# Optimization experiments

Measured on AMD Instinct MI355X. Metric: run time of the kernel, lower is better.

## Reference

```python
import jax, jax.numpy as jnp
import numpy as np

N, D, B, E = 3072, 64, 12, 49152


def _gat_conv(x, mask, W, a_src, a_dst, b):
    # PyG GATConv (eval mode): per-edge score = LeakyReLU(a_dst.Wx_i + a_src.Wx_j),
    # softmax over incoming neighbors (mask includes self-loops), concat heads.
    H, d = a_src.shape
    h = (x @ W).reshape(x.shape[0], H, d)                  # [N, H, d]
    es = jnp.einsum('nhd,hd->nh', h, a_src)                # source-side score
    ed = jnp.einsum('nhd,hd->nh', h, a_dst)                # dest-side score
    e = jax.nn.leaky_relu(ed[:, None, :] + es[None, :, :], 0.2)  # [Ndst, Nsrc, H]
    e = jnp.where(mask[:, :, None], e, -jnp.inf)
    alpha = jax.nn.softmax(e, axis=1)                      # softmax over sources
    out = jnp.einsum('ijh,jhd->ihd', alpha, h)
    return out.reshape(x.shape[0], H * d) + b


def _gcn_conv(x, Abool, W, b):
    # PyG GCNConv: add self-loops, symmetric deg^{-1/2} normalization.
    n = x.shape[0]
    Ahat = Abool.astype(x.dtype) + jnp.eye(n, dtype=x.dtype)
    deg = Ahat.sum(1)
    dinv = jnp.where(deg > 0, 1.0 / jnp.sqrt(deg), 0.0)
    return (dinv[:, None] * Ahat * dinv[None, :]) @ (x @ W) + b


def _forward(x, ei, g1_W, g1_as, g1_ad, g1_b, g2_W, g2_as, g2_ad, g2_b,
             gA_W, gA_b, gB_W, gB_b, gC_W, gC_b, c2_W, c2_b, c3_W, c3_b,
             hwA_W, hwA_b, hwB_W, hwB_b, gru_Wih, gru_Whh, gru_bih, gru_bhh,
             tA_W, tA_b, tB_W, tB_b, edge_index, atom_list, res_list):
    n = x.shape[0]
    relu = jax.nn.relu
    I = jnp.eye(n, dtype=bool)
    # A[dst, src] = 1 (PyG messages flow src -> dst); ei only sets to_dense_adj
    # values in the original, which are never used (only adj.shape).
    A = jnp.zeros((n, n), dtype=bool).at[edge_index[1], edge_index[0]].set(True)
    Af = A.astype(x.dtype)
    A2 = (Af @ Af) > 0                      # spspmm(E, E): 2-hop edges
    A3 = (Af @ A2.astype(x.dtype)) > 0      # spspmm(E^2, E): 3-hop edges
    counts = atom_list + res_list
    batch = jnp.repeat(jnp.arange(counts.shape[0]), counts, total_repeat_length=n)

    def gat_block(mask):
        v = jax.nn.elu(_gat_conv(x, mask, g1_W, g1_as, g1_ad, g1_b))
        v = relu(_gat_conv(v, mask, g2_W, g2_as, g2_ad, g2_b))
        v = relu(v @ gA_W + gA_b)
        v = relu(v @ gB_W + gB_b)
        return v @ gC_W + gC_b

    h1 = relu(gat_block(A | I))
    h1 = relu(_gcn_conv(h1, A, c2_W, c2_b))
    h1 = relu(_gcn_conv(h1, A, c3_W, c3_b))          # [N, 4D]
    h2 = relu(gat_block(A2 | I))
    h2 = relu(_gcn_conv(h2, A2, c2_W, c2_b))          # [N, 2D]
    h3 = relu(gat_block(A3 | I))                      # [N, D]
    # HighWay fusion
    bb = h2 @ hwB_W + hwB_b
    aa = h1 @ hwA_W + hwA_b
    z = jax.nn.sigmoid(aa + bb)
    hh = z * bb + (1.0 - z) * aa
    # GRUCell(input=h3, hidden=hh), PyTorch gate order r, z, n
    gx = h3 @ gru_Wih + gru_bih
    gh = hh @ gru_Whh + gru_bhh
    xr, xz, xn = jnp.split(gx, 3, axis=1)
    hr, hz, hn = jnp.split(gh, 3, axis=1)
    r = jax.nn.sigmoid(xr + hr)
    zz = jax.nn.sigmoid(xz + hz)
    nn_ = jnp.tanh(xn + r * hn)
    cc = (1.0 - zz) * nn_ + zz * hh
    vi = jax.ops.segment_max(cc, batch, num_segments=atom_list.shape[0])  # global_max_pool
    vi = relu(vi @ tA_W + tA_b)
    return vi @ tB_W + tB_b


def setup_inputs() -> dict:
    key = jax.random.key(0)
    ks = jax.random.split(key, 40)
    it = iter(range(40))

    def p(shp):
        return jax.random.normal(ks[next(it)], shp, dtype=jnp.float32) * 0.1

    src = jax.random.randint(ks[next(it)], (E,), 0, N)
    dst = jax.random.randint(ks[next(it)], (E,), 0, N)
    dst = jnp.where(dst == src, (dst + 1) % N, dst)   # no self-loops in raw edges
    edge_index = jnp.stack([src, dst])
    inp = {
        'x': jax.random.normal(ks[next(it)], (N, D), dtype=jnp.float32),
        'ei': jax.random.uniform(ks[next(it)], (E,), dtype=jnp.float32),
        'g1_W': p((D, 8 * D)), 'g1_as': p((8, D)), 'g1_ad': p((8, D)), 'g1_b': p((8 * D,)),
        'g2_W': p((8 * D, D)), 'g2_as': p((1, D)), 'g2_ad': p((1, D)), 'g2_b': p((D,)),
        'gA_W': p((D, D)), 'gA_b': p((D,)), 'gB_W': p((D, 128)), 'gB_b': p((128,)),
        'gC_W': p((128, D)), 'gC_b': p((D,)),
        'c2_W': p((D, 2 * D)), 'c2_b': p((2 * D,)), 'c3_W': p((2 * D, 4 * D)), 'c3_b': p((4 * D,)),
        'hwA_W': p((4 * D, D)), 'hwA_b': p((D,)), 'hwB_W': p((2 * D, D)), 'hwB_b': p((D,)),
        'gru_Wih': p((D, 3 * D)), 'gru_Whh': p((D, 3 * D)), 'gru_bih': p((3 * D,)), 'gru_bhh': p((3 * D,)),
        'tA_W': p((D, 128)), 'tA_b': p((128,)), 'tB_W': p((128, 120)), 'tB_b': p((120,)),
        'edge_index': edge_index,
        'atom_list': jnp.full((B,), 156, dtype=jnp.int32),
        'res_list': jnp.full((B,), 100, dtype=jnp.int32),
    }
    return inp


def reference(x, ei, g1_W, g1_as, g1_ad, g1_b, g2_W, g2_as, g2_ad, g2_b,
              gA_W, gA_b, gB_W, gB_b, gC_W, gC_b, c2_W, c2_b, c3_W, c3_b,
              hwA_W, hwA_b, hwB_W, hwB_b, gru_Wih, gru_Whh, gru_bih, gru_bhh,
              tA_W, tA_b, tB_W, tB_b, edge_index, atom_list, res_list):
    return _forward(x, ei, g1_W, g1_as, g1_ad, g1_b, g2_W, g2_as, g2_ad, g2_b,
                    gA_W, gA_b, gB_W, gB_b, gC_W, gC_b, c2_W, c2_b, c3_W, c3_b,
                    hwA_W, hwA_b, hwB_W, hwB_b, gru_Wih, gru_Whh, gru_bih, gru_bhh,
                    tA_W, tA_b, tB_W, tB_b, edge_index, atom_list, res_list)
```

## Files before the change

kernel.cpp:

```cpp
#include <hip/hip_runtime.h>
#include <math.h>

namespace {

constexpr int NN = 3072;
constexpr int NW = 96;
constexpr int NEDGE_C = 49152;
constexpr int NB = 12;
constexpr float RLN2 = 1.44269504088896340736f;

using short8v = __attribute__((ext_vector_type(8))) short;
using f32x4v  = __attribute__((ext_vector_type(4))) float;
typedef unsigned short ushort_t;

__device__ __forceinline__ float leaky02(float x) { return fmaxf(x, 0.2f * x); }
__device__ __forceinline__ float sigm(float x) { return 1.f / (1.f + __expf(-x)); }

__device__ __forceinline__ float hi_part(float a) {
  return __uint_as_float(__float_as_uint(a) & 0xffff0000u);
}
__device__ __forceinline__ unsigned pack_h(float a, float b) {
  return (__float_as_uint(a) >> 16) | (__float_as_uint(b) & 0xffff0000u);
}
__device__ __forceinline__ unsigned pack_l(float a, float b) {
// ... 175 lines not shown
                                           unsigned* jlist, int* cnt, int t) {
  if (t < 16) {
    int base = 0;
    for (int k = 0; k < t; ++k) base += __popc(rowb[p * 16 + k]);
    unsigned m = rowb[p * 16 + t];
    int j0 = p * 512 + t * 32;
    while (m) { int b = __ffs(m) - 1; m &= m - 1; jlist[base++] = j0 + b; }
    if (t == 15) *cnt = base;
  }
  __syncthreads();
  return *cnt;
}

template<int JS>
__global__ __launch_bounds__(256) void k_gat_sparse8_part(
    const float* __restrict__ hsrc,
    const float* __restrict__ es,
    const float* __restrict__ ed,
    const float* __restrict__ gm,
    const unsigned* __restrict__ bits,
    float* __restrict__ pacc,
    float* __restrict__ pden) {
  constexpr int WPS = NW / JS;
  constexpr int WPP = WPS / 2;
  __shared__ unsigned rowb[WPS];
  __shared__ unsigned jlist[WPP * 32];
  __shared__ float wl[WPP * 32 * 8];
  __shared__ int cnt;
  __shared__ float red[256];
  int i = blockIdx.x, z = blockIdx.y, t = threadIdx.x;
  int w0 = z * WPS;
  if (t < WPS) {
    unsigned wv_ = bits[(size_t)i * NW + w0 + t];
    if (w0 + t == (i >> 5)) wv_ |= 1u << (i & 31);
    rowb[t] = wv_;
  }
  int wv = t >> 6, lane = t & 63;
  int ha = lane >> 4;
  int hb = 4 + (lane >> 4);
  int ca = lane * 4;
  float4 a0 = {0.f, 0.f, 0.f, 0.f};
  float4 a1 = {0.f, 0.f, 0.f, 0.f};
  int hw = t & 7;
  float edv = ed[(size_t)i * 8 + hw];
  float mh = leaky02(edv + gm[hw]);
  float dloc = 0.f;
  __syncthreads();

  for (int p = 0; p < 2; ++p) {
    __syncthreads();
    if (t < WPP) {
      int base = 0;
      for (int k = p * WPP; k < p * WPP + t; ++k) base += __popc(rowb[k]);
      unsigned m = rowb[p * WPP + t];
      int j0 = (w0 + p * WPP + t) * 32;
      while (m) { int b = __ffs(m) - 1; m &= m - 1; jlist[base++] = j0 + b; }
      if (t == WPP - 1) cnt = base;
    }
    __syncthreads();
    int c = cnt;
    if (c == 0) continue;
    for (int pidx = t; pidx < c * 8; pidx += 256) {
      int idx = pidx >> 3;
      int j = (int)jlist[idx];
      float w = exp2f(leaky02(edv + es[(size_t)j * 8 + hw]) - mh);
      wl[idx * 8 + hw] = w;
      dloc += w;
    }
    __syncthreads();
    int idx = wv;
    for (; idx + 4 < c; idx += 8) {
      int j0 = (int)jlist[idx], j1 = (int)jlist[idx + 4];
      float w0a = wl[idx * 8 + ha],       w0b = wl[idx * 8 + hb];
      float w1a = wl[(idx + 4) * 8 + ha], w1b = wl[(idx + 4) * 8 + hb];
      float4 u0 = *(const float4*)&hsrc[(size_t)j0 * 512 + ca];
      float4 u1 = *(const float4*)&hsrc[(size_t)j0 * 512 + 256 + ca];
      float4 v0 = *(const float4*)&hsrc[(size_t)j1 * 512 + ca];
      float4 v1 = *(const float4*)&hsrc[(size_t)j1 * 512 + 256 + ca];
      a0.x += w0a * u0.x; a0.y += w0a * u0.y; a0.z += w0a * u0.z; a0.w += w0a * u0.w;
      a1.x += w0b * u1.x; a1.y += w0b * u1.y; a1.z += w0b * u1.z; a1.w += w0b * u1.w;
      a0.x += w1a * v0.x; a0.y += w1a * v0.y; a0.z += w1a * v0.z; a0.w += w1a * v0.w;
      a1.x += w1b * v1.x; a1.y += w1b * v1.y; a1.z += w1b * v1.z; a1.w += w1b * v1.w;
    }
    if (idx < c) {
      int j0 = (int)jlist[idx];
      float w0a = wl[idx * 8 + ha], w0b = wl[idx * 8 + hb];
      float4 u0 = *(const float4*)&hsrc[(size_t)j0 * 512 + ca];
      float4 u1 = *(const float4*)&hsrc[(size_t)j0 * 512 + 256 + ca];
      a0.x += w0a * u0.x; a0.y += w0a * u0.y; a0.z += w0a * u0.z; a0.w += w0a * u0.w;
      a1.x += w0b * u1.x; a1.y += w0b * u1.y; a1.z += w0b * u1.z; a1.w += w0b * u1.w;
    }
  }
  __syncthreads();
  red[t] = dloc;
  float* rbuf = wl;
  *(float4*)&rbuf[wv * 512 + ca] = a0;
  *(float4*)&rbuf[wv * 512 + 256 + ca] = a1;
  __syncthreads();
  if (t < 8) {
    float s = 0.f;
    for (int k = t; k < 256; k += 8) s += red[k];
    pden[((size_t)z * NN + i) * 8 + t] = s;
  }
  __syncthreads();
  int cc0 = 2 * t;
  float s0 = rbuf[cc0] + rbuf[512 + cc0] + rbuf[1024 + cc0] + rbuf[1536 + cc0];
  float s1 = rbuf[cc0 + 1] + rbuf[512 + cc0 + 1] + rbuf[1024 + cc0 + 1] + rbuf[1536 + cc0 + 1];
  float2 o; o.x = s0; o.y = s1;
  *(float2*)&pacc[((size_t)z * NN + i) * 512 + cc0] = o;
}

template<int ACT>
__global__ __launch_bounds__(256) void k_gat_sparse8(const float* __restrict__ hsrc,
                                                     const float* __restrict__ es,
                                                     const float* __restrict__ ed,
                                                     const float* __restrict__ gm,
                                                     const unsigned* __restrict__ bits,
                                                     const float* __restrict__ bias,
                                                     float* __restrict__ out) {
  __shared__ unsigned rowb[NW];
  __shared__ unsigned jlist[512];
  __shared__ float wl[512 * 8];
  __shared__ int cnt;
  __shared__ float red[256];
  __shared__ float sden[8];
  int i = blockIdx.x, t = threadIdx.x;
  if (t < NW) {
    unsigned wv_ = bits[(size_t)i * NW + t];
    if (t == (i >> 5)) wv_ |= 1u << (i & 31);
    rowb[t] = wv_;
  }
  int wv = t >> 6, lane = t & 63;
  int ha = lane >> 4;
  int hb = 4 + (lane >> 4);
  int ca = lane * 4;
  float4 a0 = {0.f, 0.f, 0.f, 0.f};
  float4 a1 = {0.f, 0.f, 0.f, 0.f};
  int hw = t & 7;
  float edv = ed[(size_t)i * 8 + hw];
  float mh = leaky02(edv + gm[hw]);
  float dloc = 0.f;
  __syncthreads();

  for (int p = 0; p < 6; ++p) {
    __syncthreads();
    int c = enum_bits16(rowb, p, jlist, &cnt, t);
    if (c == 0) continue;
    for (int pidx = t; pidx < c * 8; pidx += 256) {
      int idx = pidx >> 3;
      int j = (int)jlist[idx];
      float w = exp2f(leaky02(edv + es[(size_t)j * 8 + hw]) - mh);
      wl[idx * 8 + hw] = w;
      dloc += w;
    }
    __syncthreads();
    int idx = wv;
    for (; idx + 4 < c; idx += 8) {
      int j0 = (int)jlist[idx], j1 = (int)jlist[idx + 4];
      float w0a = wl[idx * 8 + ha],       w0b = wl[idx * 8 + hb];
      float w1a = wl[(idx + 4) * 8 + ha], w1b = wl[(idx + 4) * 8 + hb];
      float4 u0 = *(const float4*)&hsrc[(size_t)j0 * 512 + ca];
      float4 u1 = *(const float4*)&hsrc[(size_t)j0 * 512 + 256 + ca];
      float4 v0 = *(const float4*)&hsrc[(size_t)j1 * 512 + ca];
      float4 v1 = *(const float4*)&hsrc[(size_t)j1 * 512 + 256 + ca];
      a0.x += w0a * u0.x; a0.y += w0a * u0.y; a0.z += w0a * u0.z; a0.w += w0a * u0.w;
      a1.x += w0b * u1.x; a1.y += w0b * u1.y; a1.z += w0b * u1.z; a1.w += w0b * u1.w;
      a0.x += w1a * v0.x; a0.y += w1a * v0.y; a0.z += w1a * v0.z; a0.w += w1a * v0.w;
      a1.x += w1b * v1.x; a1.y += w1b * v1.y; a1.z += w1b * v1.z; a1.w += w1b * v1.w;
    }
    if (idx < c) {
      int j0 = (int)jlist[idx];
      float w0a = wl[idx * 8 + ha], w0b = wl[idx * 8 + hb];
      float4 u0 = *(const float4*)&hsrc[(size_t)j0 * 512 + ca];
      float4 u1 = *(const float4*)&hsrc[(size_t)j0 * 512 + 256 + ca];
      a0.x += w0a * u0.x; a0.y += w0a * u0.y; a0.z += w0a * u0.z; a0.w += w0a * u0.w;
      a1.x += w0b * u1.x; a1.y += w0b * u1.y; a1.z += w0b * u1.z; a1.w += w0b * u1.w;
    }
  }
  __syncthreads();
  red[t] = dloc;
  float* rbuf = wl;
  *(float4*)&rbuf[wv * 512 + ca] = a0;
  *(float4*)&rbuf[wv * 512 + 256 + ca] = a1;
  __syncthreads();
  if (t < 8) {
    float s = 0.f;
    for (int k = t; k < 256; k += 8) s += red[k];
    sden[t] = s;
  }
  __syncthreads();
  int cc0 = 2 * t, h2 = cc0 >> 6;
  float inv = 1.0f / sden[h2];
  float s0 = rbuf[cc0] + rbuf[512 + cc0] + rbuf[1024 + cc0] + rbuf[1536 + cc0];
  float s1 = rbuf[cc0 + 1] + rbuf[512 + cc0 + 1] + rbuf[1024 + cc0 + 1] + rbuf[1536 + cc0 + 1];
  float2 o;
  o.x = act_apply<ACT>(s0 * inv + bias[cc0]);
  o.y = act_apply<ACT>(s1 * inv + bias[cc0 + 1]);
  *(float2*)&out[(size_t)i * 512 + cc0] = o;
}

template<int ACT>
__global__ __launch_bounds__(256) void k_gat_sparse1(const float* __restrict__ hsrc,
                                                     const float* __restrict__ es,
                                                     const float* __restrict__ ed,
                                                     const float* __restrict__ gm,
                                                     const unsigned* __restrict__ bits,
                                                     const float* __restrict__ bias,
                                                     float* __restrict__ out) {
  __shared__ unsigned rowb[NW];
  __shared__ unsigned jlist[512];
  __shared__ float wl[512];
  __shared__ int cnt;
  __shared__ float red[256];
  __shared__ float red2[16 * 64];
  int i = blockIdx.x, t = threadIdx.x;
  if (t < NW) {
    unsigned wv_ = bits[(size_t)i * NW + t];
    if (t == (i >> 5)) wv_ |= 1u << (i & 31);
    rowb[t] = wv_;
  }
  int wv = t >> 6, lane = t & 63;
  int sub = lane >> 4;
  int col4 = (lane & 15) * 4;
  int g = wv * 4 + sub;
  float4 a = {0.f, 0.f, 0.f, 0.f};
  float edv = ed[i];
  float mh = leaky02(edv + gm[0]);
  float dloc = 0.f;
  __syncthreads();

  for (int p = 0; p < 6; ++p) {
    __syncthreads();
    int c = enum_bits16(rowb, p, jlist, &cnt, t);
    if (c == 0) continue;
    for (int idx = t; idx < c; idx += 256) {
      int j = (int)jlist[idx];
      float w = exp2f(leaky02(edv + es[j]) - mh);
      wl[idx] = w;
      dloc += w;
    }
    __syncthreads();
    for (int base = 0; base < c; base += 16) {
      int idx = base + g;
      if (idx < c) {
        int j = (int)jlist[idx];
        float w = wl[idx];
        float4 v = *(const float4*)&hsrc[(size_t)j * 64 + col4];
        a.x += w * v.x; a.y += w * v.y; a.z += w * v.z; a.w += w * v.w;
      }
    }
  }
  __syncthreads();
  red[t] = dloc;
  __syncthreads();
  for (int s = 128; s > 0; s >>= 1) {
    if (t < s) red[t] += red[t + s];
    __syncthreads();
  }
  float inv = 1.0f / red[0];
  *(float4*)&red2[g * 64 + col4] = a;
  __syncthreads();
  if (t < 64) {
    float s = 0.f;
    #pragma unroll
    for (int k = 0; k < 16; ++k) s += red2[k * 64 + t];
    out[(size_t)i * 64 + t] = act_apply<ACT>(s * inv + bias[t]);
  }
}

__global__ __launch_bounds__(256) void k_split_xws(const float* __restrict__ xw, int C,
                                                   const float* __restrict__ dinv,
                                                   ushort_t* __restrict__ hT,
                                                   ushort_t* __restrict__ lT) {
  __shared__ float T[64][65];
  int j0 = blockIdx.x * 64, cb0 = blockIdx.y * 64;
  int t = threadIdx.x;
  int cb = (t & 15) * 4, jrow = t >> 4;
  #pragma unroll
  for (int p = 0; p < 4; ++p) {
    int j = jrow + 16 * p;
    float dv = dinv ? dinv[j0 + j] : 1.f;
    float4 v = *(const float4*)&xw[(size_t)(j0 + j) * C + cb0 + cb];
    T[j][cb] = v.x * dv; T[j][cb + 1] = v.y * dv; T[j][cb + 2] = v.z * dv; T[j][cb + 3] = v.w * dv;
  }
  __syncthreads();
  int c = t >> 2, jq = (t & 3) * 16;
  float x[16];
  #pragma unroll
  for (int k = 0; k < 16; ++k) x[k] = T[jq + k][c];
  size_t base = ((size_t)(cb0 + c)) * NN + j0 + jq;
  uint4 u;
  u.x = pack_h(x[0], x[1]);  u.y = pack_h(x[2], x[3]);
  u.z = pack_h(x[4], x[5]);  u.w = pack_h(x[6], x[7]);
  *(uint4*)&hT[base] = u;
  u.x = pack_h(x[8], x[9]);  u.y = pack_h(x[10], x[11]);
  u.z = pack_h(x[12], x[13]); u.w = pack_h(x[14], x[15]);
  *(uint4*)&hT[base + 8] = u;
  u.x = pack_l(x[0], x[1]);  u.y = pack_l(x[2], x[3]);
  u.z = pack_l(x[4], x[5]);  u.w = pack_l(x[6], x[7]);
  *(uint4*)&lT[base] = u;
  u.x = pack_l(x[8], x[9]);  u.y = pack_l(x[10], x[11]);
  u.z = pack_l(x[12], x[13]); u.w = pack_l(x[14], x[15]);
  *(uint4*)&lT[base + 8] = u;
}

template<int H, int JS>
__global__ __launch_bounds__(256) void k_gat_dense_mfma(
    const ushort_t* __restrict__ hhT,
    const ushort_t* __restrict__ hlT,
    const float* __restrict__ es,
    const float* __restrict__ ed,
    const float* __restrict__ gm,
    const unsigned* __restrict__ bits,
    float* __restrict__ pacc,
    float* __restrict__ pden) {
  constexpr int CS = H * 64;
  constexpr int TILES = (NN / 32) / JS;
  constexpr int LW = 40;
  __shared__ ushort_t WhS[64 * LW], WlS[64 * LW];
  __shared__ ushort_t BhS[64 * LW], BlS[64 * LW];
  __shared__ float est[32];
  __shared__ unsigned mword[64];
  __shared__ float edl[64], ml[64];
  __shared__ float sred[4][64];
  int R0 = blockIdx.x * 64, hh = blockIdx.y, z = blockIdx.z;
  int t = threadIdx.x;
  int rr = t & 63, jr = t >> 6;
  int wid = t >> 6, lane = t & 63;
  int arow = lane & 15, kg = lane >> 4;
  int sc = t >> 2, sjo = (t & 3) * 8;
  const ushort_t* hhp = hhT + ((size_t)hh * 64 + sc) * NN + sjo;
  const ushort_t* hlp = hlT + ((size_t)hh * 64 + sc) * NN + sjo;
  f32x4v acc[4];
  #pragma unroll
  for (int nf = 0; nf < 4; ++nf) acc[nf] = (f32x4v){0.f, 0.f, 0.f, 0.f};
  float spart = 0.f;
  if (t < 64) {
    float e = ed[(size_t)(R0 + t) * H + hh];
    edl[t] = e;
    ml[t] = leaky02(e + gm[hh]);
  }
  int aoff = (wid * 16 + arow) * LW + kg * 8;

  for (int tt = 0; tt < TILES; ++tt) {
    int tile = z * TILES + tt, j0 = tile * 32;
    __syncthreads();
    uint4 rbh = *(const uint4*)(hhp + j0);
    uint4 rbl = *(const uint4*)(hlp + j0);
    if (t < 32) est[t] = es[(size_t)(j0 + t) * H + hh];
    if (t >= 64 && t < 128) mword[t - 64] = bits[(size_t)(R0 + t - 64) * NW + tile];
    __syncthreads();
    *(uint4*)&BhS[sc * LW + sjo] = rbh;
    *(uint4*)&BlS[sc * LW + sjo] = rbl;
    {
      unsigned wbits = mword[rr];
      int selfj = (R0 + rr) - j0;
      if (selfj >= 0 && selfj < 32) wbits |= (1u << selfj);
      float edv = edl[rr], mv = ml[rr];
      float w[8], wlo[8];
      #pragma unroll
      for (int q = 0; q < 8; ++q) {
        int jj = jr * 8 + q;
        float v = 0.f;
        if (wbits & (1u << jj)) v = exp2f(leaky02(edv + est[jj]) - mv);
        w[q] = v;
        spart += v;
        wlo[q] = v - hi_part(v);
      }
      uint4 uh, ul;
      uh.x = pack_h(w[0], w[1]); uh.y = pack_h(w[2], w[3]);
      uh.z = pack_h(w[4], w[5]); uh.w = pack_h(w[6], w[7]);
      ul.x = pack_h(wlo[0], wlo[1]); ul.y = pack_h(wlo[2], wlo[3]);
      ul.z = pack_h(wlo[4], wlo[5]); ul.w = pack_h(wlo[6], wlo[7]);
      *(uint4*)&WhS[rr * LW + jr * 8] = uh;
      *(uint4*)&WlS[rr * LW + jr * 8] = ul;
    }
    __syncthreads();
    short8v Ah = *(const short8v*)&WhS[aoff];
    short8v Al = *(const short8v*)&WlS[aoff];
    #pragma unroll
    for (int nf = 0; nf < 4; ++nf) {
      short8v bh = *(const short8v*)&BhS[(nf * 16 + arow) * LW + kg * 8];
      short8v bl = *(const short8v*)&BlS[(nf * 16 + arow) * LW + kg * 8];
      acc[nf] = __builtin_amdgcn_mfma_f32_16x16x32_bf16(Ah, bh, acc[nf], 0, 0, 0);
      acc[nf] = __builtin_amdgcn_mfma_f32_16x16x32_bf16(Ah, bl, acc[nf], 0, 0, 0);
      acc[nf] = __builtin_amdgcn_mfma_f32_16x16x32_bf16(Al, bh, acc[nf], 0, 0, 0);
    }
  }
  __syncthreads();
  sred[jr][rr] = spart;
  __syncthreads();
  if (t < 64)
    pden[((size_t)z * NN + R0 + t) * H + hh] =
        sred[0][t] + sred[1][t] + sred[2][t] + sred[3][t];
  #pragma unroll
  for (int nf = 0; nf < 4; ++nf) {
    #pragma unroll
    for (int r = 0; r < 4; ++r) {
      int row = R0 + wid * 16 + kg * 4 + r;
      int c = hh * 64 + nf * 16 + arow;
      pacc[((size_t)z * NN + row) * CS + c] = acc[nf][r];
    }
  }
}

template<int H, int ACT, int JS>
__global__ __launch_bounds__(256) void k_gat_dense_red(const float* __restrict__ pacc,
                                                       const float* __restrict__ pden,
                                                       const float* __restrict__ bias,
                                                       float* __restrict__ out) {
  constexpr int CS = H * 64;
  int idx = blockIdx.x * 256 + threadIdx.x;
  if (idx >= NN * CS) return;
  int row = idx / CS, c = idx - row * CS, hh = c >> 6;
  float a = 0.f, d = 0.f;
  #pragma unroll
  for (int z = 0; z < JS; ++z) a += pacc[((size_t)z * NN + row) * CS + c];
  #pragma unroll
  for (int z = 0; z < JS; ++z) d += pden[((size_t)z * NN + row) * H + hh];
  out[idx] = act_apply<ACT>(a / d + bias[c]);
}

template<int H, int ACT>
__global__ __launch_bounds__(256) void k_gat_dense(const float* __restrict__ hsrc,
                                                   const float* __restrict__ es,
                                                   const float* __restrict__ ed,
                                                   const float* __restrict__ gm,
                                                   const unsigned* __restrict__ bits,
                                                   const float* __restrict__ bias,
                                                   float* __restrict__ out) {
  constexpr int CS = H * 64;
  __shared__ float htile[32][68];
  __shared__ float wl[32][68];
  __shared__ float est[32];
  __shared__ unsigned mword[64];
  __shared__ float edl[64], ml[64];
  __shared__ float sred[4][64];
  int R0 = blockIdx.x * 64;
  int hh = blockIdx.y;
  int t = threadIdx.x;
  int rg = t >> 4, dg = t & 15;
  int rr = t & 63, jr = t >> 6;
  float acc[4][4] = {{0.f}};
  float spart = 0.f;
  if (t < 64) {
    float e = ed[(size_t)(R0 + t) * H + hh];
    edl[t] = e;
    ml[t] = leaky02(e + gm[hh]);
  }
  __syncthreads();
  for (int tile = 0; tile < NN / 32; ++tile) {
    int j0 = tile * 32;
    {
      int jj = t >> 3, cq = (t & 7) * 8;
      const float* hp = hsrc + (size_t)(j0 + jj) * CS + hh * 64 + cq;
      *(float4*)&htile[jj][cq]     = *(const float4*)hp;
      *(float4*)&htile[jj][cq + 4] = *(const float4*)(hp + 4);
    }
    if (t < 32) est[t] = es[(size_t)(j0 + t) * H + hh];
    if (t >= 64 && t < 128) mword[t - 64] = bits[(size_t)(R0 + t - 64) * NW + tile];
    __syncthreads();
    {
      unsigned wbits = mword[rr];
      int selfj = (R0 + rr) - j0;
      if (selfj >= 0 && selfj < 32) wbits |= (1u << selfj);
      float edv = edl[rr], mv = ml[rr];
      #pragma unroll
      for (int q = 0; q < 8; ++q) {
        int jj = (q << 2) | jr;
        float w = 0.f;
        if (wbits & (1u << jj)) {
          w = exp2f(leaky02(edv + est[jj]) - mv);
        }
        wl[jj][rr] = w;
        spart += w;
      }
    }
    __syncthreads();
    #pragma unroll 8
    for (int jj = 0; jj < 32; ++jj) {
      float4 av = *(const float4*)&wl[jj][rg * 4];
      float4 bv = *(const float4*)&htile[jj][dg * 4];
      float ar[4] = {av.x, av.y, av.z, av.w};
      float br[4] = {bv.x, bv.y, bv.z, bv.w};
      #pragma unroll
      for (int ri = 0; ri < 4; ++ri)
        #pragma unroll
        for (int ci = 0; ci < 4; ++ci)
          acc[ri][ci] += ar[ri] * br[ci];
    }
    __syncthreads();
  }
  sred[jr][rr] = spart;
  __syncthreads();
  if (t < 64) ml[t] = sred[0][t] + sred[1][t] + sred[2][t] + sred[3][t];
  __syncthreads();
  int cbase = hh * 64 + dg * 4;
  float bv0 = bias[cbase], bv1 = bias[cbase + 1], bv2 = bias[cbase + 2], bv3 = bias[cbase + 3];
  for (int ri = 0; ri < 4; ++ri) {
    int r = rg * 4 + ri;
    float inv = 1.0f / ml[r];
    float4 o;
    o.x = act_apply<ACT>(acc[ri][0] * inv + bv0);
    o.y = act_apply<ACT>(acc[ri][1] * inv + bv1);
    o.z = act_apply<ACT>(acc[ri][2] * inv + bv2);
    o.w = act_apply<ACT>(acc[ri][3] * inv + bv3);
    *(float4*)&out[(size_t)(R0 + r) * CS + cbase] = o;
  }
}

template<int JS>
__global__ __launch_bounds__(256) void k_gcn_mfma(
    const ushort_t* __restrict__ bhT,
    const ushort_t* __restrict__ blT,
    const unsigned* __restrict__ b0,
    const unsigned* __restrict__ b1,
    float* __restrict__ pacc,
    int zRows, int rowOffY, int colOffY, int cStride) {
  constexpr int TILES = (NN / 32) / JS;
  constexpr int LW = 40;
  __shared__ ushort_t BhS[128 * LW], BlS[128 * LW];
  __shared__ unsigned mword[64];
  int R0 = blockIdx.x * 64, y = blockIdx.y, z = blockIdx.z;
  const unsigned* bits = y ? b1 : b0;
  int t = threadIdx.x;
  int wid = t >> 6, lane = t & 63;
  int arow = lane & 15, kg = lane >> 4;
  int sc = t >> 1, jh = (t & 1) * 16;
  const ushort_t* bhp = bhT + ((size_t)y * 128 + sc) * NN + jh;
  const ushort_t* blp = blT + ((size_t)y * 128 + sc) * NN + jh;
  f32x4v acc[4][2];
  #pragma unroll
  for (int rf = 0; rf < 4; ++rf)
    #pragma unroll
    for (int cf = 0; cf < 2; ++cf) acc[rf][cf] = (f32x4v){0.f, 0.f, 0.f, 0.f};

  for (int tt = 0; tt < TILES; ++tt) {
    int tile = z * TILES + tt, j0 = tile * 32;
    uint4 h0 = *(const uint4*)(bhp + j0);
    uint4 h1 = *(const uint4*)(bhp + j0 + 8);
    uint4 l0 = *(const uint4*)(blp + j0);
    uint4 l1 = *(const uint4*)(blp + j0 + 8);
    __syncthreads();
    *(uint4*)&BhS[sc * LW + jh]     = h0;
    *(uint4*)&BhS[sc * LW + jh + 8] = h1;
    *(uint4*)&BlS[sc * LW + jh]     = l0;
    *(uint4*)&BlS[sc * LW + jh + 8] = l1;
    if (t < 64) mword[t] = bits[(size_t)(R0 + t) * NW + tile];
    __syncthreads();
    short8v Aw[4];
    #pragma unroll
    for (int rf = 0; rf < 4; ++rf) {
      unsigned wb = mword[rf * 16 + arow];
      unsigned oct = (wb >> (kg * 8)) & 0xffu;
      #pragma unroll
      for (int q = 0; q < 8; ++q)
        Aw[rf][q] = (short)(((oct >> q) & 1u) ? 0x3f80 : 0);
    }
    #pragma unroll
    for (int cf = 0; cf < 2; ++cf) {
      int col = wid * 32 + cf * 16 + arow;
      short8v bh = *(const short8v*)&BhS[col * LW + kg * 8];
      short8v bl = *(const short8v*)&BlS[col * LW + kg * 8];
      #pragma unroll
      for (int rf = 0; rf < 4; ++rf) {
        acc[rf][cf] = __builtin_amdgcn_mfma_f32_16x16x32_bf16(Aw[rf], bh, acc[rf][cf], 0, 0, 0);
        acc[rf][cf] = __builtin_amdgcn_mfma_f32_16x16x32_bf16(Aw[rf], bl, acc[rf][cf], 0, 0, 0);
      }
    }
  }
  #pragma unroll
  for (int rf = 0; rf < 4; ++rf)
    #pragma unroll
    for (int cf = 0; cf < 2; ++cf)
      #pragma unroll
      for (int r = 0; r < 4; ++r) {
        int row = R0 + rf * 16 + kg * 4 + r;
        int c = wid * 32 + cf * 16 + arow;
        pacc[((size_t)z * zRows + (size_t)y * rowOffY + row) * cStride + y * colOffY + c] =
            acc[rf][cf][r];
      }
}

template<int JS>
__global__ __launch_bounds__(256) void k_gcn_red(const float* __restrict__ pacc,
                                                 const float* __restrict__ xw,
                                                 const float* __restrict__ d0,
                                                 const float* __restrict__ d1,
                                                 const float* __restrict__ bias,
                                                 float* __restrict__ out,
                                                 int rowsTotal, int C) {
  int idx = blockIdx.x * 256 + threadIdx.x;
  if (idx >= rowsTotal * C) return;
  int blk = idx / C, c = idx - blk * C;
  float s = 0.f;
  #pragma unroll
  for (int z = 0; z < JS; ++z) s += pacc[((size_t)z * rowsTotal + blk) * C + c];
  int i = blk >= NN ? blk - NN : blk;
  float di = (blk >= NN ? d1 : d0)[i];
  float v = di * (s + di * xw[(size_t)blk * C + c]) + bias[c];
  out[idx] = fmaxf(v, 0.f);
}

__global__ __launch_bounds__(256) void k_gcn256(const float* __restrict__ xw,
                                                const unsigned* __restrict__ bits,
                                                const float* __restrict__ dinv,
                                                const float* __restrict__ bias,
                                                float* __restrict__ out) {
  __shared__ unsigned rowb[NW];
  __shared__ unsigned jlist[512];
  __shared__ int cnt;
  int i = blockIdx.x, t = threadIdx.x;
  if (t < NW) rowb[t] = bits[(size_t)i * NW + t];
  float acc = 0.f;
  __syncthreads();
  for (int p = 0; p < 6; ++p) {
    __syncthreads();
    int cN = enum_bits16(rowb, p, jlist, &cnt, t);
    for (int idx = 0; idx < cN; ++idx) {
      int j = (int)jlist[idx];
      acc += dinv[j] * xw[(size_t)j * 256 + t];
    }
  }
  float di = dinv[i];
  float v = di * (acc + di * xw[(size_t)i * 256 + t]) + bias[t];
  out[(size_t)i * 256 + t] = fmaxf(v, 0.f);
}

__global__ __launch_bounds__(256) void k_gcn128b(const float* __restrict__ xw,
                                                 const unsigned* __restrict__ b0,
                                                 const unsigned* __restrict__ b1,
                                                 const float* __restrict__ d0,
                                                 const float* __restrict__ d1,
                                                 const float* __restrict__ bias,
                                                 float* __restrict__ outb) {
  __shared__ unsigned rowb[NW];
  __shared__ unsigned jlist[512];
  __shared__ int cnt;
  __shared__ float red[256];
  int blk = blockIdx.x, t = threadIdx.x;
  int br = blk >= NN;
  int i = br ? blk - NN : blk;
  const unsigned* bits = br ? b1 : b0;
  const float* dinv = br ? d1 : d0;
  const float* xb = xw + (size_t)br * NN * 128;
  if (t < NW) rowb[t] = bits[(size_t)i * NW + t];
  int g = t >> 7, c = t & 127;
  float acc = 0.f;
  __syncthreads();
  for (int p = 0; p < 6; ++p) {
    __syncthreads();
    int cN = enum_bits16(rowb, p, jlist, &cnt, t);
    for (int idx = g; idx < cN; idx += 2) {
      int j = (int)jlist[idx];
      acc += dinv[j] * xb[(size_t)j * 128 + c];
    }
  }
  __syncthreads();
  red[t] = acc;
  __syncthreads();
  if (t < 128) {
    acc = red[t] + red[t + 128];
    float di = dinv[i];
    float v = di * (acc + di * xb[(size_t)i * 128 + c]) + bias[c];
    outb[(size_t)blk * 128 + c] = fmaxf(v, 0.f);
  }
}

__global__ __launch_bounds__(256) void k_highway(const float* __restrict__ aa,
                                                 const float* __restrict__ bb,
                                                 float* __restrict__ hh) {
  int idx = blockIdx.x * 256 + threadIdx.x;
  if (idx < NN * 64) {
    float a = aa[idx], b = bb[idx];
    float z = sigm(a + b);
    hh[idx] = z * b + (1.f - z) * a;
  }
}

__global__ __launch_bounds__(256) void k_gru(const float* __restrict__ gx,
                                             const float* __restrict__ gh,
                                             const float* __restrict__ hh,
                                             float* __restrict__ cc) {
  int idx = blockIdx.x * 256 + threadIdx.x;
  if (idx < NN * 64) {
    int i = idx >> 6, d = idx & 63;
    float xr = gx[(size_t)i * 192 + d];
    float xz = gx[(size_t)i * 192 + 64 + d];
    float xn = gx[(size_t)i * 192 + 128 + d];
    float hr = gh[(size_t)i * 192 + d];
    float hz = gh[(size_t)i * 192 + 64 + d];
    float hn = gh[(size_t)i * 192 + 128 + d];
    float r = sigm(xr + hr);
    float z = sigm(xz + hz);
    float n = tanhf(xn + r * hn);
    cc[idx] = (1.f - z) * n + z * hh[idx];
  }
}

__global__ __launch_bounds__(64) void k_pool(const float* __restrict__ cc,
                                             const int* __restrict__ atoms,
                                             const int* __restrict__ resl,
                                             float* __restrict__ vi) {
  int s = blockIdx.x, lane = threadIdx.x;
  int start = 0;
  for (int k = 0; k < s; ++k) start += atoms[k] + resl[k];
  int end = start + atoms[s] + resl[s];
  if (end > NN) end = NN;
  float m = -3.0e38f;
  for (int r = start; r < end; ++r) m = fmaxf(m, cc[(size_t)r * 64 + lane]);
  vi[s * 64 + lane] = m;
}

__global__ __launch_bounds__(256) void k_final(const float* __restrict__ vi,
                                               const float* __restrict__ tAW,
                                               const float* __restrict__ tAb,
                                               const float* __restrict__ tBW,
                                               const float* __restrict__ tBb,
                                               float* __restrict__ out) {
  __shared__ float v[NB * 64];
  __shared__ float t1[NB * 128];
  int t = threadIdx.x;
  for (int idx = t; idx < NB * 64; idx += 256) v[idx] = vi[idx];
  __syncthreads();
  for (int idx = t; idx < NB * 128; idx += 256) {
    int r = idx >> 7, c = idx & 127;
    float a = tAb[c];
    for (int k = 0; k < 64; ++k) a += v[r * 64 + k] * tAW[k * 128 + c];
    t1[idx] = fmaxf(a, 0.f);
  }
  __syncthreads();
  for (int idx = t; idx < NB * 120; idx += 256) {
    int r = idx / 120, c = idx % 120;
    float a = tBb[c];
    for (int k = 0; k < 128; ++k) a += t1[r * 128 + k] * tBW[k * 120 + c];
    out[idx] = a;
  }
}

}

extern "C" void kernel_launch(void* const* d_in, const int* in_sizes, int n_in,
                              void* d_out, int out_size, void* d_ws, size_t ws_size,
                              hipStream_t stream) {
  (void)in_sizes; (void)n_in; (void)out_size;
  const float* x     = (const float*)d_in[0];
  const float* g1_W  = (const float*)d_in[2];
  const float* g1_as = (const float*)d_in[3];
  const float* g1_ad = (const float*)d_in[4];
  const float* g1_b  = (const float*)d_in[5];
  const float* g2_W  = (const float*)d_in[6];
  const float* g2_as = (const float*)d_in[7];
  const float* g2_ad = (const float*)d_in[8];
  const float* g2_b  = (const float*)d_in[9];
  const float* gA_W  = (const float*)d_in[10];
  const float* gA_b  = (const float*)d_in[11];
  const float* gB_W  = (const float*)d_in[12];
  const float* gB_b  = (const float*)d_in[13];
  const float* gC_W  = (const float*)d_in[14];
  const float* gC_b  = (const float*)d_in[15];
  const float* c2_W  = (const float*)d_in[16];
  const float* c2_b  = (const float*)d_in[17];
  const float* c3_W  = (const float*)d_in[18];
  const float* c3_b  = (const float*)d_in[19];
  const float* hwA_W = (const float*)d_in[20];
  const float* hwA_b = (const float*)d_in[21];
  const float* hwB_W = (const float*)d_in[22];
  const float* hwB_b = (const float*)d_in[23];
  const float* gWih  = (const float*)d_in[24];
  const float* gWhh  = (const float*)d_in[25];
  const float* gbih  = (const float*)d_in[26];
  const float* gbhh  = (const float*)d_in[27];
  const float* tA_W  = (const float*)d_in[28];
  const float* tA_b  = (const float*)d_in[29];
  const float* tB_W  = (const float*)d_in[30];
  const float* tB_b  = (const float*)d_in[31];
  const int* edges   = (const int*)d_in[32];
  const int* atoms   = (const int*)d_in[33];
  const int* resl    = (const int*)d_in[34];
  float* out = (float*)d_out;

  unsigned* bitsA  = (unsigned*)d_ws;
  unsigned* bitsA2 = bitsA + (size_t)NN * NW;
  unsigned* bitsA3 = bitsA2 + (size_t)NN * NW;
  float* fp = (float*)(bitsA3 + (size_t)NN * NW);
  float* dinvA  = fp; fp += NN;
  float* dinvA2 = fp; fp += NN;
  float* HB     = fp; fp += (size_t)NN * 512;
  float* ES1    = fp; fp += (size_t)NN * 8;
  float* ED1    = fp; fp += (size_t)NN * 8;
  float* GM1    = fp; fp += 16;
  float* V1ALL  = fp; fp += (size_t)3 * NN * 512;
  float* H2BALL = fp; fp += (size_t)3 * NN * 64;
  float* ES2ALL = fp; fp += (size_t)3 * NN;
  float* ED2ALL = fp; fp += (size_t)3 * NN;
  float* GM2ALL = fp; fp += 16;
  float* V2ALL  = fp; fp += (size_t)3 * NN * 64;
  float* V3ALL  = fp; fp += (size_t)3 * NN * 64;
  float* V4ALL  = fp; fp += (size_t)3 * NN * 128;
  float* V5ALL  = fp; fp += (size_t)3 * NN * 64;
  float* XC2    = fp; fp += (size_t)2 * NN * 128;
  float* TG     = fp; fp += (size_t)2 * NN * 128;
  float* XC3    = fp; fp += (size_t)NN * 256;
  float* H1F    = fp; fp += (size_t)NN * 256;
  float* AAb    = fp; fp += (size_t)NN * 64;
  float* BBb    = fp; fp += (size_t)NN * 64;
  float* HHb    = fp; fp += (size_t)NN * 64;
  float* VI     = fp; fp += NB * 64;
  float* GX = V1ALL;
  float* GH = V1ALL + (size_t)NN * 192;
  float* CC = V1ALL + (size_t)NN * 384;
  char* cp = (char*)fp;
  ushort_t* HhT8 = (ushort_t*)cp; cp += (size_t)512 * NN * 2;
  ushort_t* HlT8 = (ushort_t*)cp; cp += (size_t)512 * NN * 2;
  ushort_t* HhT1 = (ushort_t*)cp; cp += (size_t)64 * NN * 2;
  ushort_t* HlT1 = (ushort_t*)cp; cp += (size_t)64 * NN * 2;
  ushort_t* XWSH = (ushort_t*)cp; cp += (size_t)256 * NN * 2;
  ushort_t* XWSL = (ushort_t*)cp; cp += (size_t)256 * NN * 2;
  float* PACC = (float*)cp; cp += (size_t)4 * NN * 512 * 4;
  float* PDEN = (float*)cp; cp += (size_t)16 * NN * 8 * 4;
  int mode = ((size_t)(cp - (char*)d_ws) <= ws_size) ? 1 : 0;

  float* H3F = V5ALL + (size_t)2 * NN * 64;
  float* H2F = TG + (size_t)NN * 128;

  hipMemsetAsync(bitsA, 0, (size_t)NN * NW * sizeof(unsigned), stream);
  k_scatter<<<(NEDGE_C + 255) / 256, 256, 0, stream>>>(edges, bitsA);
  k_bmm<<<NN, 128, 0, stream>>>(bitsA, bitsA, bitsA2);
  k_bmm<<<NN, 128, 0, stream>>>(bitsA, bitsA2, bitsA3);
  k_dinv<<<NN / 256, 256, 0, stream>>>(bitsA, dinvA);
  k_dinv<<<NN / 256, 256, 0, stream>>>(bitsA2, dinvA2);

  k_gemm<0><<<dim3(48, 8), 256, 0, stream>>>(x, g1_W, nullptr, HB, 64, 512);
  k_scores<8><<<NN, 64, 0, stream>>>(HB, g1_as, g1_ad, ES1, ED1);
  k_gmax8<<<1, 256, 0, stream>>>(ES1, GM1);

  if (mode) {
    k_gat_sparse8_part<4><<<dim3(NN, 4), 256, 0, stream>>>(HB, ES1, ED1, GM1, bitsA, PACC, PDEN);
    k_gat_dense_red<8, 2, 4><<<NN * 512 / 256, 256, 0, stream>>>(PACC, PDEN, g1_b, V1ALL);
    k_gat_sparse8_part<4><<<dim3(NN, 4), 256, 0, stream>>>(HB, ES1, ED1, GM1, bitsA2, PACC, PDEN);
    k_gat_dense_red<8, 2, 4><<<NN * 512 / 256, 256, 0, stream>>>(PACC, PDEN, g1_b, V1ALL + (size_t)NN * 512);
    k_split_xws<<<dim3(48, 8), 256, 0, stream>>>(HB, 512, nullptr, HhT8, HlT8);
    k_gat_dense_mfma<8, 4><<<dim3(48, 8, 4), 256, 0, stream>>>(HhT8, HlT8, ES1, ED1, GM1, bitsA3, PACC, PDEN);
    k_gat_dense_red<8, 2, 4><<<NN * 512 / 256, 256, 0, stream>>>(PACC, PDEN, g1_b, V1ALL + (size_t)2 * NN * 512);
  } else {
    k_gat_sparse8<2><<<NN, 256, 0, stream>>>(HB, ES1, ED1, GM1, bitsA, g1_b, V1ALL);
    k_gat_sparse8<2><<<NN, 256, 0, stream>>>(HB, ES1, ED1, GM1, bitsA2, g1_b, V1ALL + (size_t)NN * 512);
    k_gat_dense<8, 2><<<dim3(48, 8), 256, 0, stream>>>(HB, ES1, ED1, GM1, bitsA3, g1_b, V1ALL + (size_t)2 * NN * 512);
  }

  k_gemm<0><<<dim3(144, 1), 256, 0, stream>>>(V1ALL, g2_W, nullptr, H2BALL, 512, 64);
  k_scores<1><<<3 * NN, 64, 0, stream>>>(H2BALL, g2_as, g2_ad, ES2ALL, ED2ALL);
  k_gmax1b<<<3, 256, 0, stream>>>(ES2ALL, GM2ALL);

  k_gat_sparse1<1><<<NN, 256, 0, stream>>>(H2BALL, ES2ALL, ED2ALL, GM2ALL, bitsA, g2_b, V2ALL);
  k_gat_sparse1<1><<<NN, 256, 0, stream>>>(H2BALL + (size_t)NN * 64, ES2ALL + NN, ED2ALL + NN,
                                           GM2ALL + 1, bitsA2, g2_b, V2ALL + (size_t)NN * 64);
  if (mode) {
    k_split_xws<<<dim3(48, 1), 256, 0, stream>>>(H2BALL + (size_t)2 * NN * 64, 64, nullptr, HhT1, HlT1);
    k_gat_dense_mfma<1, 16><<<dim3(48, 1, 16), 256, 0, stream>>>(
        HhT1, HlT1, ES2ALL + 2 * NN, ED2ALL + 2 * NN, GM2ALL + 2, bitsA3, PACC, PDEN);
    k_gat_dense_red<1, 1, 16><<<NN * 64 / 256, 256, 0, stream>>>(PACC, PDEN, g2_b, V2ALL + (size_t)2 * NN * 64);
  } else {
    k_gat_dense<1, 1><<<dim3(48, 1), 256, 0, stream>>>(
        H2BALL + (size_t)2 * NN * 64, ES2ALL + 2 * NN, ED2ALL + 2 * NN, GM2ALL + 2, bitsA3, g2_b,
        V2ALL + (size_t)2 * NN * 64);
  }

  k_gemm<1><<<dim3(144, 1), 256, 0, stream>>>(V2ALL, gA_W, gA_b, V3ALL, 64, 64);
  k_gemm<1><<<dim3(144, 2), 256, 0, stream>>>(V3ALL, gB_W, gB_b, V4ALL, 64, 128);
  k_gemm<1><<<dim3(144, 1), 256, 0, stream>>>(V4ALL, gC_W, gC_b, V5ALL, 128, 64);

  k_gemm<0><<<dim3(96, 2), 256, 0, stream>>>(V5ALL, c2_W, nullptr, XC2, 64, 128);
  if (mode) {
    k_split_xws<<<dim3(48, 2), 256, 0, stream>>>(XC2, 128, dinvA, XWSH, XWSL);
    k_split_xws<<<dim3(48, 2), 256, 0, stream>>>(XC2 + (size_t)NN * 128, 128, dinvA2,
                                                 XWSH + (size_t)128 * NN, XWSL + (size_t)128 * NN);
    k_gcn_mfma<8><<<dim3(48, 2, 8), 256, 0, stream>>>(XWSH, XWSL, bitsA, bitsA2, PACC, 2 * NN, NN, 0, 128);
    k_gcn_red<8><<<2 * NN * 128 / 256, 256, 0, stream>>>(PACC, XC2, dinvA, dinvA2, c2_b, TG, 2 * NN, 128);
  } else {
    k_gcn128b<<<2 * NN, 256, 0, stream>>>(XC2, bitsA, bitsA2, dinvA, dinvA2, c2_b, TG);
  }
  k_gemm<0><<<dim3(48, 4), 256, 0, stream>>>(TG, c3_W, nullptr, XC3, 128, 256);
  if (mode) {
    k_split_xws<<<dim3(48, 4), 256, 0, stream>>>(XC3, 256, dinvA, XWSH, XWSL);
    k_gcn_mfma<8><<<dim3(48, 2, 8), 256, 0, stream>>>(XWSH, XWSL, bitsA, bitsA, PACC, NN, 0, 128, 256);
    k_gcn_red<8><<<NN * 256 / 256, 256, 0, stream>>>(PACC, XC3, dinvA, dinvA, c3_b, H1F, NN, 256);
  } else {
    k_gcn256<<<NN, 256, 0, stream>>>(XC3, bitsA, dinvA, c3_b, H1F);
  }

  k_gemm<0><<<dim3(48, 1), 256, 0, stream>>>(H1F, hwA_W, hwA_b, AAb, 256, 64);
  k_gemm<0><<<dim3(48, 1), 256, 0, stream>>>(H2F, hwB_W, hwB_b, BBb, 128, 64);
  k_highway<<<NN * 64 / 256, 256, 0, stream>>>(AAb, BBb, HHb);
  k_gemm<0><<<dim3(48, 3), 256, 0, stream>>>(H3F, gWih, gbih, GX, 64, 192);
  k_gemm<0><<<dim3(48, 3), 256, 0, stream>>>(HHb, gWhh, gbhh, GH, 64, 192);
  k_gru<<<NN * 64 / 256, 256, 0, stream>>>(GX, GH, HHb, CC);
  k_pool<<<NB, 64, 0, stream>>>(CC, atoms, resl, VI);
  k_final<<<1, 256, 0, stream>>>(VI, tA_W, tA_b, tB_W, tB_b, out);
}
```

Measured before the change: 585.7 us.

## Add 128-thread 64-row-tile MFMA kernel for layer-1 3-hop dense GAT

Adds a specialised dense GAT attention kernel for the 8-head layer-1 3-hop pass. Each block handles 64 destination rows with 2 waves, stages 64-source tiles of bf16 hi/lo features and softmax weights in XOR-swizzled shared memory, and uses 16x16x32 bf16 MFMA with three-term split precision. It also merges the two waves' partial sums in shared memory before writing. The aim is more reuse per block and fewer LDS bank conflicts than the previous 256-thread kernel, at the cost of more registers and shared memory per block. The new kernel only runs when mode is set.

Measured after the change: 619.4 us. +5.8%, slower.

```diff
diff --git a/kernel.cpp b/kernel.cpp
--- a/kernel.cpp
+++ b/kernel.cpp
@@ -501,6 +501,147 @@
   u.x = pack_l(x[8], x[9]);  u.y = pack_l(x[10], x[11]);
   u.z = pack_l(x[12], x[13]); u.w = pack_l(x[14], x[15]);
   *(uint4*)&lT[base + 8] = u;
+}
+
+__global__ __launch_bounds__(128) void k_gat_dense_mfma_w64(
+    const ushort_t* __restrict__ hhT,
+    const ushort_t* __restrict__ hlT,
+    const float* __restrict__ es,
+    const float* __restrict__ ed,
+    const float* __restrict__ gm,
+    const unsigned* __restrict__ bits,
+    float* __restrict__ pacc,
+    float* __restrict__ pden) {
+  __shared__ __align__(16) unsigned char SMEM[33536];
+  ushort_t* WhS = (ushort_t*)SMEM;
+  ushort_t* WlS = (ushort_t*)(SMEM + 8192);
+  ushort_t* BhS = (ushort_t*)(SMEM + 16384);
+  ushort_t* BlS = (ushort_t*)(SMEM + 24576);
+  float* est  = (float*)(SMEM + 32768);
+  float* sden = (float*)(SMEM + 33024);
+
+  int R0 = blockIdx.x * 64, hh = blockIdx.y, z = blockIdx.z;
+  int t = threadIdx.x;
+  int wv = t >> 6, lane = t & 63;
+  int arow = lane & 15, kg = lane >> 4;
+  int row = t & 63, jq = t >> 6;
+  int scol = t >> 1, sp = t & 1;
+  float edv = ed[(size_t)(R0 + row) * 8 + hh];
+  float mh = leaky02(edv + gm[hh]);
+  float spart = 0.f;
+  f32x4v acc[4][4];
+  #pragma unroll
+  for (int s = 0; s < 4; ++s)
+    #pragma unroll
+    for (int cf = 0; cf < 4; ++cf) acc[s][cf] = (f32x4v){0.f, 0.f, 0.f, 0.f};
+  const ushort_t* hhp = hhT + ((size_t)(hh * 64 + scol)) * NN + sp * 32;
+  const ushort_t* hlp = hlT + ((size_t)(hh * 64 + scol)) * NN + sp * 32;
+  int bswz = (scol & 7) << 3;
+  int wswz = (row & 7) << 3;
+  int rswz = (arow & 7) << 3;
+
+  for (int sup = 0; sup < 12; ++sup) {
+    int j0 = z * 768 + sup * 64;
+    __syncthreads();
+    if (t < 64) est[t] = es[(size_t)(j0 + t) * 8 + hh];
+    uint4 b0 = *(const uint4*)(hhp + j0);
+    uint4 b1 = *(const uint4*)(hhp + j0 + 8);
+    uint4 b2 = *(const uint4*)(hhp + j0 + 16);
+    uint4 b3 = *(const uint4*)(hhp + j0 + 24);
+    uint4 c0 = *(const uint4*)(hlp + j0);
+    uint4 c1 = *(const uint4*)(hlp + j0 + 8);
+    uint4 c2 = *(const uint4*)(hlp + j0 + 16);
+    uint4 c3 = *(const uint4*)(hlp + j0 + 24);
+    unsigned wb = bits[(size_t)(R0 + row) * NW + (j0 >> 5) + jq];
+    {
+      int sl = (R0 + row) - (j0 + jq * 32);
+      if (sl >= 0 && sl < 32) wb |= 1u << sl;
+    }
+    {
+      int bb = scol * 64;
+      *(uint4*)&BhS[bb + ((sp * 32 + 0)  ^ bswz)] = b0;
+      *(uint4*)&BhS[bb + ((sp * 32 + 8)  ^ bswz)] = b1;
+      *(uint4*)&BhS[bb + ((sp * 32 + 16) ^ bswz)] = b2;
+      *(uint4*)&BhS[bb + ((sp * 32 + 24) ^ bswz)] = b3;
+      *(uint4*)&BlS[bb + ((sp * 32 + 0)  ^ bswz)] = c0;
+      *(uint4*)&BlS[bb + ((sp * 32 + 8)  ^ bswz)] = c1;
+      *(uint4*)&BlS[bb + ((sp * 32 + 16) ^ bswz)] = c2;
+      *(uint4*)&BlS[bb + ((sp * 32 + 24) ^ bswz)] = c3;
+    }
+    __syncthreads();
+    #pragma unroll
+    for (int g = 0; g < 4; ++g) {
+      float w[8], wlo[8];
+      #pragma unroll
+      for (int q = 0; q < 8; ++q) {
+        int jj = jq * 32 + g * 8 + q;
+        float v = 0.f;
+        if (wb & (1u << (g * 8 + q))) v = exp2f(leaky02(edv + est[jj]) - mh);
+        w[q] = v;
+        spart += v;
+        wlo[q] = v - hi_part(v);
+      }
+      uint4 uh, ul;
+      uh.x = pack_h(w[0], w[1]); uh.y = pack_h(w[2], w[3]);
+      uh.z = pack_h(w[4], w[5]); uh.w = pack_h(w[6], w[7]);
+      ul.x = pack_h(wlo[0], wlo[1]); ul.y = pack_h(wlo[2], wlo[3]);
+      ul.z = pack_h(wlo[4], wlo[5]); ul.w = pack_h(wlo[6], wlo[7]);
+      int off = row * 64 + ((jq * 32 + g * 8) ^ wswz);
+      *(uint4*)&WhS[off] = uh;
+      *(uint4*)&WlS[off] = ul;
+    }
+    __syncthreads();
+    int ju = (wv * 32 + kg * 8) ^ rswz;
+    short8v Bh_[4], Bl_[4];
+    #pragma unroll
+    for (int cf = 0; cf < 4; ++cf) {
+      Bh_[cf] = *(const short8v*)&BhS[(cf * 16 + arow) * 64 + ju];
+      Bl_[cf] = *(const short8v*)&BlS[(cf * 16 + arow) * 64 + ju];
+    }
+    #pragma unroll
+    for (int s = 0; s < 4; ++s) {
+      short8v Ah = *(const short8v*)&WhS[(s * 16 + arow) * 64 + ju];
+      short8v Al = *(const short8v*)&WlS[(s * 16 + arow) * 64 + ju];
+      #pragma unroll
+      for (int cf = 0; cf < 4; ++cf) {
+        acc[s][cf] = __builtin_amdgcn_mfma_f32_16x16x32_bf16(Ah, Bh_[cf], acc[s][cf], 0, 0, 0);
+        acc[s][cf] = __builtin_amdgcn_mfma_f32_16x16x32_bf16(Ah, Bl_[cf], acc[s][cf], 0, 0, 0);
+        acc[s][cf] = __builtin_amdgcn_mfma_f32_16x16x32_bf16(Al, Bh_[cf], acc[s][cf], 0, 0, 0);
+      }
+    }
+  }
+  sden[jq * 64 + row] = spart;
+  __syncthreads();
+  if (t < 64)
+    pden[((size_t)z * NN + R0 + t) * 8 + hh] = sden[t] + sden[64 + t];
+  float* rb = (float*)SMEM;
+  {
+    float* rbw = rb + wv * 4096;
+    #pragma unroll
+    for (int s = 0; s < 4; ++s)
+      #pragma unroll
+      for (int cf = 0; cf < 4; ++cf)
+        #pragma unroll
+        for (int r = 0; r < 4; ++r)
+          rbw[(s * 16 + kg * 4 + r) * 64 + (((cf ^ r) * 16) + arow)] = acc[s][cf][r];
+  }
+  __syncthreads();
+  {
+    int rrow = t >> 1, cb = (t & 1) * 32;
+    int sw = (rrow & 3) << 4;
+    float* dst = &pacc[((size_t)z * NN + R0 + rrow) * 512 + hh * 64 + cb];
+    const float* r0 = rb + rrow * 64;
+    const float* r1 = r0 + 4096;
+    #pragma unroll
+    for (int q = 0; q < 8; ++q) {
+      int c = (cb + q * 4) ^ sw;
+      float4 a = *(const float4*)(r0 + c);
+      float4 b = *(const float4*)(r1 + c);
+      float4 o;
+      o.x = a.x + b.x; o.y = a.y + b.y; o.z = a.z + b.z; o.w = a.w + b.w;
+      *(float4*)(dst + q * 4) = o;
+    }
+  }
 }
 
 template<int H, int JS>
@@ -1040,7 +1181,7 @@
     k_gat_sparse8_part<4><<<dim3(NN, 4), 256, 0, stream>>>(HB, ES1, ED1, GM1, bitsA2, PACC, PDEN);
     k_gat_dense_red<8, 2, 4><<<NN * 512 / 256, 256, 0, stream>>>(PACC, PDEN, g1_b, V1ALL + (size_t)NN * 512);
     k_split_xws<<<dim3(48, 8), 256, 0, stream>>>(HB, 512, nullptr, HhT8, HlT8);
-    k_gat_dense_mfma<8, 4><<<dim3(48, 8, 4), 256, 0, stream>>>(HhT8, HlT8, ES1, ED1, GM1, bitsA3, PACC, PDEN);
+    k_gat_dense_mfma_w64<<<dim3(48, 8, 4), 128, 0, stream>>>(HhT8, HlT8, ES1, ED1, GM1, bitsA3, PACC, PDEN);
     k_gat_dense_red<8, 2, 4><<<NN * 512 / 256, 256, 0, stream>>>(PACC, PDEN, g1_b, V1ALL + (size_t)2 * NN * 512);
   } else {
     k_gat_sparse8<2><<<NN, 256, 0, stream>>>(HB, ES1, ED1, GM1, bitsA, g1_b, V1ALL);
```

## Prefetch next tile in GAT dense kernel and load mask and score per thread

Applied to the files above, without the earlier changes.

Restructures the dense GAT MFMA loop so the B-tile global loads for the next tile are issued before the MFMAs of the current tile (register double buffering). The shared-memory staging of es, ed, mask words and max is dropped: each thread reads its own mask word and es values straight from global memory. This cuts one barrier per tile and hides global load latency behind compute. In exchange there are more redundant global loads per thread, mostly served from cache, and more register pressure.

Measured after the change: 626.3 us. 6.9% more time.

```diff
diff --git a/kernel.cpp b/kernel.cpp
--- a/kernel.cpp
+++ b/kernel.cpp
@@ -518,9 +518,6 @@
   constexpr int LW = 40;
   __shared__ ushort_t WhS[64 * LW], WlS[64 * LW];
   __shared__ ushort_t BhS[64 * LW], BlS[64 * LW];
-  __shared__ float est[32];
-  __shared__ unsigned mword[64];
-  __shared__ float edl[64], ml[64];
   __shared__ float sred[4][64];
   int R0 = blockIdx.x * 64, hh = blockIdx.y, z = blockIdx.z;
   int t = threadIdx.x;
@@ -530,49 +527,48 @@
   int sc = t >> 2, sjo = (t & 3) * 8;
   const ushort_t* hhp = hhT + ((size_t)hh * 64 + sc) * NN + sjo;
   const ushort_t* hlp = hlT + ((size_t)hh * 64 + sc) * NN + sjo;
+  const unsigned* wrow = bits + (size_t)(R0 + rr) * NW;
   f32x4v acc[4];
   #pragma unroll
   for (int nf = 0; nf < 4; ++nf) acc[nf] = (f32x4v){0.f, 0.f, 0.f, 0.f};
   float spart = 0.f;
-  if (t < 64) {
-    float e = ed[(size_t)(R0 + t) * H + hh];
-    edl[t] = e;
-    ml[t] = leaky02(e + gm[hh]);
-  }
+  float edv = ed[(size_t)(R0 + rr) * H + hh];
+  float mh = leaky02(edv + gm[hh]);
   int aoff = (wid * 16 + arow) * LW + kg * 8;
+  int jbase = z * TILES * 32;
+  uint4 rbh = *(const uint4*)(hhp + jbase);
+  uint4 rbl = *(const uint4*)(hlp + jbase);
 
   for (int tt = 0; tt < TILES; ++tt) {
-    int tile = z * TILES + tt, j0 = tile * 32;
-    __syncthreads();
-    uint4 rbh = *(const uint4*)(hhp + j0);
-    uint4 rbl = *(const uint4*)(hlp + j0);
-    if (t < 32) est[t] = es[(size_t)(j0 + t) * H + hh];
-    if (t >= 64 && t < 128) mword[t - 64] = bits[(size_t)(R0 + t - 64) * NW + tile];
+    int j0 = jbase + tt * 32;
+    unsigned wb = wrow[j0 >> 5];
+    {
+      int sl = (R0 + rr) - j0;
+      if (sl >= 0 && sl < 32) wb |= 1u << sl;
+    }
+    float w[8], wlo[8];
+    #pragma unroll
+    for (int q = 0; q < 8; ++q) {
+      int jj = jr * 8 + q;
+      float esv = es[(size_t)(j0 + jj) * H + hh];
+      float v = (wb & (1u << jj)) ? exp2f(leaky02(edv + esv) - mh) : 0.f;
+      w[q] = v;
+      spart += v;
+      wlo[q] = v - hi_part(v);
+    }
+    uint4 uh, ul;
+    uh.x = pack_h(w[0], w[1]); uh.y = pack_h(w[2], w[3]);
+    uh.z = pack_h(w[4], w[5]); uh.w = pack_h(w[6], w[7]);
+    ul.x = pack_h(wlo[0], wlo[1]); ul.y = pack_h(wlo[2], wlo[3]);
+    ul.z = pack_h(wlo[4], wlo[5]); ul.w = pack_h(wlo[6], wlo[7]);
     __syncthreads();
     *(uint4*)&BhS[sc * LW + sjo] = rbh;
     *(uint4*)&BlS[sc * LW + sjo] = rbl;
-    {
-      unsigned wbits = mword[rr];
-      int selfj = (R0 + rr) - j0;
-      if (selfj >= 0 && selfj < 32) wbits |= (1u << selfj);
-      float edv = edl[rr], mv = ml[rr];
-      float w[8], wlo[8];
-      #pragma unroll
-      for (int q = 0; q < 8; ++q) {
-        int jj = jr * 8 + q;
-        float v = 0.f;
-        if (wbits & (1u << jj)) v = exp2f(leaky02(edv + est[jj]) - mv);
-        w[q] = v;
-        spart += v;
-        wlo[q] = v - hi_part(v);
-      }
-      uint4 uh, ul;
-      uh.x = pack_h(w[0], w[1]); uh.y = pack_h(w[2], w[3]);
-      uh.z = pack_h(w[4], w[5]); uh.w = pack_h(w[6], w[7]);
-      ul.x = pack_h(wlo[0], wlo[1]); ul.y = pack_h(wlo[2], wlo[3]);
-      ul.z = pack_h(wlo[4], wlo[5]); ul.w = pack_h(wlo[6], wlo[7]);
-      *(uint4*)&WhS[rr * LW + jr * 8] = uh;
-      *(uint4*)&WlS[rr * LW + jr * 8] = ul;
+    *(uint4*)&WhS[rr * LW + jr * 8] = uh;
+    *(uint4*)&WlS[rr * LW + jr * 8] = ul;
+    if (tt + 1 < TILES) {
+      rbh = *(const uint4*)(hhp + j0 + 32);
+      rbl = *(const uint4*)(hlp + j0 + 32);
     }
     __syncthreads();
     short8v Ah = *(const short8v*)&WhS[aoff];
@@ -586,7 +582,6 @@
       acc[nf] = __builtin_amdgcn_mfma_f32_16x16x32_bf16(Al, bh, acc[nf], 0, 0, 0);
     }
   }
-  __syncthreads();
   sred[jr][rr] = spart;
   __syncthreads();
   if (t < 64)
```
